# Optimization experiments

Measured on AMD Instinct MI355X. Metric: run time of the kernel, lower is better.

Reference implementation:

```python
import jax, jax.numpy as jnp
import numpy as np
from jax import lax

T, B, IN, H = 512, 64, 1024, 2048


def setup_inputs() -> dict:
    key = jax.random.key(0)
    k1, k2, k3, k4, k5, k6 = jax.random.split(key, 6)
    inputs = jax.random.normal(k1, (T, B, IN), dtype=jnp.float32) * 0.1
    hidden = jax.random.normal(k2, (1, B, H), dtype=jnp.float32) * 0.1
    # i2h params (default nn.Linear init ~ small); h2h initialised per irnn_initializer
    Wi = jax.random.normal(k3, (H, IN), dtype=jnp.float32) * 0.02
    bi = jax.random.normal(k4, (H,), dtype=jnp.float32) * 0.01
    Wh = jnp.eye(H, dtype=jnp.float32) + jax.random.normal(k5, (H, H), dtype=jnp.float32) * 0.005
    bh = jax.random.normal(k6, (H,), dtype=jnp.float32) * 0.01
    return {"inputs": inputs, "hidden": hidden, "Wi": Wi, "bi": bi, "Wh": Wh, "bh": bh}


def reference(inputs, hidden, Wi, bi, Wh, bh):
    h0 = hidden[0]  # [B, H]
    # Precompute the input projection for all timesteps in one big GEMM
    x_proj = jnp.einsum('tbi,hi->tbh', inputs, Wi) + bi  # [T, B, H]

    def step(h, xp):
        h = jax.nn.relu(h @ Wh.T + bh + xp)
        return h, h

    h_last, outputs = lax.scan(step, h0, x_proj)
    return outputs, h_last[None]  # ([T,B,H], [1,B,H])
```

## Files before the change

kernel.cpp:

```cpp
#include <hip/hip_runtime.h>

#define T_DIM 512
#define B_DIM 64
#define IN_DIM 1024
#define H_DIM 2048
#define BH (B_DIM * H_DIM)
#define KT 64
#define KC (H_DIM / KT)

__global__ __launch_bounds__(256) void irnn_xproj(
    const float* __restrict__ A, const float* __restrict__ Wi,
    const float* __restrict__ bi, const float* __restrict__ bh,
    float* __restrict__ out)
{
  __shared__ float As[32][132];
  __shared__ float Bs[32][132];
  const int tid = threadIdx.x;
  const int tx = tid & 15;
  const int ty = tid >> 4;
  const size_t row0 = (size_t)blockIdx.x * 128;
  const int    col0 = blockIdx.y * 128;
  float acc[8][8] = {};

  for (int k0 = 0; k0 < IN_DIM; k0 += 32) {
    #pragma unroll
    for (int i = 0; i < 4; ++i) {
      int f = tid + 256 * i;
      int r = f >> 3, c = f & 7;
      const float4 v = *reinterpret_cast<const float4*>(
          A + (row0 + r) * IN_DIM + k0 + c * 4);
      As[c*4+0][r] = v.x; As[c*4+1][r] = v.y;
      As[c*4+2][r] = v.z; As[c*4+3][r] = v.w;
    }
    #pragma unroll
    for (int i = 0; i < 4; ++i) {
      int f = tid + 256 * i;
      int r = f >> 3, c = f & 7;
      const float4 v = *reinterpret_cast<const float4*>(
          Wi + (size_t)(col0 + r) * IN_DIM + k0 + c * 4);
      Bs[c*4+0][r] = v.x; Bs[c*4+1][r] = v.y;
      Bs[c*4+2][r] = v.z; Bs[c*4+3][r] = v.w;
    }
    __syncthreads();
    #pragma unroll
    for (int k = 0; k < 32; ++k) {
      float a[8], b[8];
      #pragma unroll
      for (int i = 0; i < 8; i += 4)
        *reinterpret_cast<float4*>(&a[i]) =
            *reinterpret_cast<const float4*>(&As[k][ty*8 + i]);
      #pragma unroll
      for (int j = 0; j < 8; j += 4)
        *reinterpret_cast<float4*>(&b[j]) =
            *reinterpret_cast<const float4*>(&Bs[k][tx*8 + j]);
      #pragma unroll
      for (int i = 0; i < 8; ++i)
        #pragma unroll
        for (int j = 0; j < 8; ++j)
          acc[i][j] = fmaf(a[i], b[j], acc[i][j]);
    }
    __syncthreads();
  }

  float bias[8];
  #pragma unroll
  for (int j = 0; j < 8; j += 4) {
    float4 v1 = *reinterpret_cast<const float4*>(bi + col0 + tx*8 + j);
    float4 v2 = *reinterpret_cast<const float4*>(bh + col0 + tx*8 + j);
    bias[j+0] = v1.x + v2.x; bias[j+1] = v1.y + v2.y;
    bias[j+2] = v1.z + v2.z; bias[j+3] = v1.w + v2.w;
  }
  #pragma unroll
  for (int i = 0; i < 8; ++i) {
    size_t o = (row0 + ty*8 + i) * H_DIM + col0 + tx*8;
    #pragma unroll
    for (int j = 0; j < 8; j += 4) {
      float4 v;
      v.x = acc[i][j+0] + bias[j+0];
      v.y = acc[i][j+1] + bias[j+1];
      v.z = acc[i][j+2] + bias[j+2];
      v.w = acc[i][j+3] + bias[j+3];
      *reinterpret_cast<float4*>(out + o + j) = v;
    }
  }
}

__global__ __launch_bounds__(256) void irnn_transpose(
    const float* __restrict__ Wh, float* __restrict__ WhT)
{
  __shared__ float tile[64][68];
  const int tid = threadIdx.x;
  const int j0 = blockIdx.x * 64;
  const int k0 = blockIdx.y * 64;
  #pragma unroll
  for (int i = 0; i < 4; ++i) {
    int f = tid + 256 * i;
    int r = f >> 4, cq = f & 15;
    float4 v = *reinterpret_cast<const float4*>(
        Wh + (size_t)(j0 + r) * H_DIM + k0 + cq * 4);
    *reinterpret_cast<float4*>(&tile[r][cq*4]) = v;
  }
  __syncthreads();
  #pragma unroll
  for (int i = 0; i < 4; ++i) {
    int f = tid + 256 * i;
    int r2 = f >> 4, c2 = f & 15;
    float4 v;
    v.x = tile[c2*4+0][r2];
    v.y = tile[c2*4+1][r2];
    v.z = tile[c2*4+2][r2];
    v.w = tile[c2*4+3][r2];
    *reinterpret_cast<float4*>(WhT + (size_t)(k0 + r2) * H_DIM + j0 + c2*4) = v;
  }
}

__global__ __launch_bounds__(256) void irnn_step_gemm(
    const float* __restrict__ h_prev,
    const float* __restrict__ WhT,
    float* __restrict__ P)
{
  const int tid = threadIdx.x;
  const int tn = tid & 31;
  const int tm = tid >> 5;
  const int jt = blockIdx.x;
  const int kt = blockIdx.y;
  const int kc = kt * KC;
  const float* hp = h_prev + kc;
  const float* wp = WhT + (size_t)kc * H_DIM + jt * 256 + tn * 4;
  float acc[8][8] = {};

  #pragma unroll
  for (int kg = 0; kg < KC / 4; ++kg) {
    float4 hv[8];
    #pragma unroll
    for (int u = 0; u < 4; ++u) {
      hv[u]   = *reinterpret_cast<const float4*>(
          hp + (size_t)(4*tm + u) * H_DIM + kg * 4);
      hv[4+u] = *reinterpret_cast<const float4*>(
          hp + (size_t)(32 + 4*tm + u) * H_DIM + kg * 4);
    }
    float4 wv0[4], wv1[4];
    #pragma unroll
    for (int kk = 0; kk < 4; ++kk) {
      wv0[kk] = *reinterpret_cast<const float4*>(wp + (size_t)(kg*4 + kk) * H_DIM);
      wv1[kk] = *reinterpret_cast<const float4*>(wp + (size_t)(kg*4 + kk) * H_DIM + 128);
    }
    #pragma unroll
    for (int kk = 0; kk < 4; ++kk) {
      #pragma unroll
      for (int r = 0; r < 8; ++r) {
        const float hs = reinterpret_cast<const float*>(&hv[r])[kk];
        acc[r][0] = fmaf(hs, wv0[kk].x, acc[r][0]);
        acc[r][1] = fmaf(hs, wv0[kk].y, acc[r][1]);
        acc[r][2] = fmaf(hs, wv0[kk].z, acc[r][2]);
        acc[r][3] = fmaf(hs, wv0[kk].w, acc[r][3]);
        acc[r][4] = fmaf(hs, wv1[kk].x, acc[r][4]);
        acc[r][5] = fmaf(hs, wv1[kk].y, acc[r][5]);
        acc[r][6] = fmaf(hs, wv1[kk].z, acc[r][6]);
        acc[r][7] = fmaf(hs, wv1[kk].w, acc[r][7]);
      }
    }
  }

  float* pb = P + (size_t)kt * BH + jt * 256 + tn * 4;
  #pragma unroll
  for (int r = 0; r < 8; ++r) {
    const int row = (r >> 2) * 32 + 4*tm + (r & 3);
    float4 v0; v0.x = acc[r][0]; v0.y = acc[r][1]; v0.z = acc[r][2]; v0.w = acc[r][3];
    float4 v1; v1.x = acc[r][4]; v1.y = acc[r][5]; v1.z = acc[r][6]; v1.w = acc[r][7];
    *reinterpret_cast<float4*>(pb + (size_t)row * H_DIM)       = v0;
    *reinterpret_cast<float4*>(pb + (size_t)row * H_DIM + 128) = v1;
  }
}

__global__ __launch_bounds__(128) void irnn_reduce(
    const float4* __restrict__ P4,
    float4* __restrict__ xp_out,
    float4* __restrict__ h_last)
{
  const int o4 = blockIdx.x * 128 + threadIdx.x;
  float4 a = xp_out[o4];
  float sx = 0.f, sy = 0.f, sz = 0.f, sw = 0.f;
  #pragma unroll 8
  for (int kt = 0; kt < KT; ++kt) {
    const float4 p = P4[(size_t)kt * (BH/4) + o4];
    sx += p.x; sy += p.y; sz += p.z; sw += p.w;
  }
  a.x = fmaxf(a.x + sx, 0.f);
  a.y = fmaxf(a.y + sy, 0.f);
  a.z = fmaxf(a.z + sz, 0.f);
  a.w = fmaxf(a.w + sw, 0.f);
  xp_out[o4] = a;
  if (h_last) h_last[o4] = a;
}

extern "C" void kernel_launch(void* const* d_in, const int* in_sizes, int n_in,
                              void* d_out, int out_size, void* d_ws, size_t ws_size,
                              hipStream_t stream) {
  const float* inputs = (const float*)d_in[0];
  const float* hidden = (const float*)d_in[1];
  const float* Wi     = (const float*)d_in[2];
  const float* bi     = (const float*)d_in[3];
  const float* Wh     = (const float*)d_in[4];
  const float* bh     = (const float*)d_in[5];
  float* out = (float*)d_out;

  float* scratch = (ws_size >= (size_t)48 * 1024 * 1024)
                       ? (float*)d_ws : (float*)d_in[0];
  float* P   = scratch;
  float* WhT = scratch + (size_t)8 * 1024 * 1024;

  irnn_xproj<<<dim3(256, 16), 256, 0, stream>>>(inputs, Wi, bi, bh, out);
  irnn_transpose<<<dim3(32, 32), 256, 0, stream>>>(Wh, WhT);

  for (int t = 0; t < T_DIM; ++t) {
    const float* hp = (t == 0) ? hidden : out + (size_t)(t - 1) * BH;
    irnn_step_gemm<<<dim3(8, KT), 256, 0, stream>>>(hp, WhT, P);
    float4* hl = (t == T_DIM - 1)
                     ? (float4*)(out + (size_t)T_DIM * BH) : nullptr;
    irnn_reduce<<<dim3(256), 128, 0, stream>>>(
        (const float4*)P, (float4*)(out + (size_t)t * BH), hl);
  }
}
```

Baseline: 14.28 ms.

## Retile recurrent step GEMM: fewer K splits, more column tiles, smaller per-thread tile

The per-timestep h@Wh^T kernel now splits K into 16 chunks instead of 64 and uses 32 column tiles of 64 instead of 8 tiles of 256. Each thread computes a 4x4 output tile rather than 8x8. This cuts the partial-sum buffer and the reduce kernel's reads fourfold, and lowers register pressure. The cost is less register-level reuse per thread and a longer K loop per block.

```diff
diff --git a/kernel.cpp b/kernel.cpp
--- a/kernel.cpp
+++ b/kernel.cpp
@@ -5,8 +5,9 @@
 #define IN_DIM 1024
 #define H_DIM 2048
 #define BH (B_DIM * H_DIM)
-#define KT 64
+#define KT 16
 #define KC (H_DIM / KT)
+#define JT 32
 
 __global__ __launch_bounds__(256) void irnn_xproj(
     const float* __restrict__ A, const float* __restrict__ Wi,
@@ -120,57 +121,42 @@
     float* __restrict__ P)
 {
   const int tid = threadIdx.x;
-  const int tn = tid & 31;
-  const int tm = tid >> 5;
+  const int tn = tid & 15;
+  const int tm = tid >> 4;
   const int jt = blockIdx.x;
   const int kt = blockIdx.y;
   const int kc = kt * KC;
-  const float* hp = h_prev + kc;
-  const float* wp = WhT + (size_t)kc * H_DIM + jt * 256 + tn * 4;
-  float acc[8][8] = {};
-
-  #pragma unroll
+  const float* hp = h_prev + (size_t)(tm * 4) * H_DIM + kc;
+  const float* wp = WhT + (size_t)kc * H_DIM + jt * 64 + tn * 4;
+  float4 acc[4] = {};
+
+  #pragma unroll 4
   for (int kg = 0; kg < KC / 4; ++kg) {
-    float4 hv[8];
+    float4 hv[4], wv[4];
+    #pragma unroll
+    for (int u = 0; u < 4; ++u)
+      hv[u] = *reinterpret_cast<const float4*>(hp + (size_t)u * H_DIM + kg * 4);
+    #pragma unroll
+    for (int kk = 0; kk < 4; ++kk)
+      wv[kk] = *reinterpret_cast<const float4*>(wp + (size_t)(kg * 4 + kk) * H_DIM);
     #pragma unroll
     for (int u = 0; u < 4; ++u) {
-      hv[u]   = *reinterpret_cast<const float4*>(
-          hp + (size_t)(4*tm + u) * H_DIM + kg * 4);
-      hv[4+u] = *reinterpret_cast<const float4*>(
-          hp + (size_t)(32 + 4*tm + u) * H_DIM + kg * 4);
-    }
-    float4 wv0[4], wv1[4];
-    #pragma unroll
-    for (int kk = 0; kk < 4; ++kk) {
-      wv0[kk] = *reinterpret_cast<const float4*>(wp + (size_t)(kg*4 + kk) * H_DIM);
-      wv1[kk] = *reinterpret_cast<const float4*>(wp + (size_t)(kg*4 + kk) * H_DIM + 128);
-    }
-    #pragma unroll
-    for (int kk = 0; kk < 4; ++kk) {
-      #pragma unroll
-      for (int r = 0; r < 8; ++r) {
-        const float hs = reinterpret_cast<const float*>(&hv[r])[kk];
-        acc[r][0] = fmaf(hs, wv0[kk].x, acc[r][0]);
-        acc[r][1] = fmaf(hs, wv0[kk].y, acc[r][1]);
-        acc[r][2] = fmaf(hs, wv0[kk].z, acc[r][2]);
-        acc[r][3] = fmaf(hs, wv0[kk].w, acc[r][3]);
-        acc[r][4] = fmaf(hs, wv1[kk].x, acc[r][4]);
-        acc[r][5] = fmaf(hs, wv1[kk].y, acc[r][5]);
-        acc[r][6] = fmaf(hs, wv1[kk].z, acc[r][6]);
-        acc[r][7] = fmaf(hs, wv1[kk].w, acc[r][7]);
+      const float* hu = reinterpret_cast<const float*>(&hv[u]);
+      #pragma unroll
+      for (int kk = 0; kk < 4; ++kk) {
+        const float hs = hu[kk];
+        acc[u].x = fmaf(hs, wv[kk].x, acc[u].x);
+        acc[u].y = fmaf(hs, wv[kk].y, acc[u].y);
+        acc[u].z = fmaf(hs, wv[kk].z, acc[u].z);
+        acc[u].w = fmaf(hs, wv[kk].w, acc[u].w);
       }
     }
   }
 
-  float* pb = P + (size_t)kt * BH + jt * 256 + tn * 4;
-  #pragma unroll
-  for (int r = 0; r < 8; ++r) {
-    const int row = (r >> 2) * 32 + 4*tm + (r & 3);
-    float4 v0; v0.x = acc[r][0]; v0.y = acc[r][1]; v0.z = acc[r][2]; v0.w = acc[r][3];
-    float4 v1; v1.x = acc[r][4]; v1.y = acc[r][5]; v1.z = acc[r][6]; v1.w = acc[r][7];
-    *reinterpret_cast<float4*>(pb + (size_t)row * H_DIM)       = v0;
-    *reinterpret_cast<float4*>(pb + (size_t)row * H_DIM + 128) = v1;
-  }
+  float* pb = P + (size_t)kt * BH + (size_t)(tm * 4) * H_DIM + jt * 64 + tn * 4;
+  #pragma unroll
+  for (int u = 0; u < 4; ++u)
+    *reinterpret_cast<float4*>(pb + (size_t)u * H_DIM) = acc[u];
 }
 
 __global__ __launch_bounds__(128) void irnn_reduce(
@@ -181,9 +167,9 @@
   const int o4 = blockIdx.x * 128 + threadIdx.x;
   float4 a = xp_out[o4];
   float sx = 0.f, sy = 0.f, sz = 0.f, sw = 0.f;
-  #pragma unroll 8
+  #pragma unroll
   for (int kt = 0; kt < KT; ++kt) {
-    const float4 p = P4[(size_t)kt * (BH/4) + o4];
+    const float4 p = P4[(size_t)kt * (BH / 4) + o4];
     sx += p.x; sy += p.y; sz += p.z; sw += p.w;
   }
   a.x = fmaxf(a.x + sx, 0.f);
@@ -205,17 +191,17 @@
   const float* bh     = (const float*)d_in[5];
   float* out = (float*)d_out;
 
-  float* scratch = (ws_size >= (size_t)48 * 1024 * 1024)
+  float* scratch = (ws_size >= (size_t)24 * 1024 * 1024)
                        ? (float*)d_ws : (float*)d_in[0];
   float* P   = scratch;
-  float* WhT = scratch + (size_t)8 * 1024 * 1024;
+  float* WhT = scratch + (size_t)2 * 1024 * 1024;
 
   irnn_xproj<<<dim3(256, 16), 256, 0, stream>>>(inputs, Wi, bi, bh, out);
   irnn_transpose<<<dim3(32, 32), 256, 0, stream>>>(Wh, WhT);
 
   for (int t = 0; t < T_DIM; ++t) {
     const float* hp = (t == 0) ? hidden : out + (size_t)(t - 1) * BH;
-    irnn_step_gemm<<<dim3(8, KT), 256, 0, stream>>>(hp, WhT, P);
+    irnn_step_gemm<<<dim3(JT, KT), 256, 0, stream>>>(hp, WhT, P);
     float4* hl = (t == T_DIM - 1)
                      ? (float4*)(out + (size_t)T_DIM * BH) : nullptr;
     irnn_reduce<<<dim3(256), 128, 0, stream>>>(
```

Result: slower. 14.86 ms (+4.1%).
